# Kernel optimization log

Hardware: AMD Instinct MI355X
Metric: run time of the kernel (lower is better)

Reference implementation:

```python
import jax, jax.numpy as jnp
import numpy as np

# ContextualAttention config (matches init_kwargs)
KS, STRIDE, DIL, FUSE_K, SCALE = 3, 1, 1, 3, 10.0
B, C, H, W = 2, 128, 64, 64
L = H * W  # number of background patches (SAME padding, stride 1)


def _same_pad(x, k, s):
    # TF-style SAME padding, identical to the repo's same_padding helper
    _, _, h, w = x.shape
    oh, ow = -(-h // s), -(-w // s)
    ph = max(0, (oh - 1) * s + k - h)
    pw = max(0, (ow - 1) * s + k - w)
    return jnp.pad(x, ((0, 0), (0, 0), (ph // 2, ph - ph // 2), (pw // 2, pw - pw // 2)))


def _patches(x, k, s):
    # extract_image_patches: SAME pad + unfold -> [N, L, C*k*k], (c, kh, kw) ordering
    xp = _same_pad(x, k, s)
    n, c, hp, wp = xp.shape
    oh, ow = (hp - k) // s + 1, (wp - k) // s + 1
    cols = jnp.stack(
        [xp[:, :, i:i + (oh - 1) * s + 1:s, j:j + (ow - 1) * s + 1:s]
         for i in range(k) for j in range(k)], axis=2)  # [N, C, k*k, oh, ow]
    return cols.reshape(n, c * k * k, oh * ow).transpose(0, 2, 1)


def _fuse(scores):
    # diagonal fuse-smoothing: conv the [L_b, L_f] score matrix with eye(k), twice
    # (second pass on the transposed spatial layout), exactly as in the torch code
    bn = scores.shape[0]
    eye = jnp.eye(FUSE_K, dtype=scores.dtype)[None, None]  # [1,1,k,k]
    conv = lambda v: jax.lax.conv_general_dilated(
        v, eye, (1, 1), [(1, 1), (1, 1)],
        dimension_numbers=('NCHW', 'OIHW', 'NCHW'))
    y = conv(scores.reshape(bn, 1, L, L))
    y = y.reshape(bn, H, W, H, W).transpose(0, 2, 1, 4, 3).reshape(bn, 1, L, L)
    y = conv(y)
    y = y.reshape(bn, W, H, W, H).transpose(0, 2, 1, 4, 3)  # back to [b,H,W,H,W]
    return y.reshape(bn, L, H, W)


def setup_inputs() -> dict:
    key = jax.random.key(0)
    kf, kb, km = jax.random.split(key, 3)
    f = jax.random.normal(kf, (B, C, H, W), jnp.float32)
    b = jax.random.normal(kb, (B, C, H, W), jnp.float32)
    mask = (jax.random.uniform(km, (1, 1, H, W)) < 0.05).astype(jnp.float32)
    return {"f": f, "b": b, "mask": mask}


def reference(f, b, mask):
    kernel = 2 * DIL  # raw patch size for aggregation (=2)
    # raw background patches used by the transposed-conv aggregation
    raw_w = _patches(b, kernel, DIL * STRIDE).reshape(B, L, C, kernel, kernel)
    # DIL == 1 => F.interpolate(scale=1.0, nearest) is identity on f/b/mask
    w = _patches(b, KS, STRIDE)      # [B, L, C*9] matching patches
    fp = _patches(f, KS, 1)          # [B, Lf, C*9] foreground patches (SAME pad)
    m = _patches(mask, KS, STRIDE)[0]                    # [L, 9]
    mm = (jnp.mean(m, axis=1) == 0.0).astype(f.dtype)    # [L] 1 = patch usable

    # per-patch L2 normalization (clamped at 1e-4), conv-as-similarity == patch GEMM
    wn = w / jnp.maximum(jnp.sqrt(jnp.sum(w * w, axis=2, keepdims=True)), 1e-4)
    scores = jnp.einsum('bkd,bqd->bkq', wn, fp).reshape(B, L, H, W)
    scores = _fuse(scores)

    mmb = mm[None, :, None, None]
    attn = jax.nn.softmax(scores * mmb * SCALE, axis=1) * mmb  # softmax over L

    # conv_transpose2d(attn, raw_w, stride=1, padding=1) == VALID corr with flipped,
    # IO-swapped 2x2 kernel (k-1-p = 0 padding); per-sample weights -> vmap
    def agg(a, rw):  # a: [L,H,W], rw: [L,C,2,2]
        rhs = jnp.flip(rw, axis=(2, 3)).transpose(1, 0, 2, 3)  # [C, L, 2, 2] OIHW
        return jax.lax.conv_general_dilated(
            a[None], rhs, (1, 1), [(0, 0), (0, 0)],
            dimension_numbers=('NCHW', 'OIHW', 'NCHW'))[0]

    y = jax.vmap(agg)(attn, raw_w) / 4.0       # [B, C, H-1, W-1]
    y = jnp.pad(y, ((0, 0), (0, 0), (0, 1), (0, 1)))  # output_padding = DIL % 2 = 1
    return y
```

## Files before the change

### kernel.cpp

```cpp
#include <hip/hip_runtime.h>

#define L 4096
#define HH 64
#define CC 128
#define BB 2

typedef _Float16 f16;
typedef _Float16 f16x8 __attribute__((ext_vector_type(8)));
typedef float f32x4 __attribute__((ext_vector_type(4)));

__device__ __forceinline__ void gl_lds16(const f16* g, f16* l) {
  __builtin_amdgcn_global_load_lds(
      (const __attribute__((address_space(1))) void*)g,
      (__attribute__((address_space(3))) void*)l, 16, 0, 0);
}

__device__ __forceinline__ int sigma_(int j) { return ((j & 63) << 6) | (j >> 6); }

__device__ float fuse9(const f16* __restrict__ Sb, int k, int j) {
  float acc = 0.f;
  int cK = sigma_(k), cQ = sigma_(j);
#pragma unroll
  for (int u = -1; u <= 1; ++u) {
    int a = cK + u, bq = cQ + u;
    if ((unsigned)a < L && (unsigned)bq < L) {
      int r = sigma_(a), c = sigma_(bq);
#pragma unroll
      for (int t = -1; t <= 1; ++t) {
        int rr = r + t, cc = c + t;
        if ((unsigned)rr < L && (unsigned)cc < L) acc += (float)Sb[(size_t)rr * L + cc];
      }
    }
  }
  return acc;
}

__global__ __launch_bounds__(256) void k_repack(
    const float* __restrict__ b, const float* __restrict__ f,
    f16* __restrict__ bT, f16* __restrict__ fT, f16* __restrict__ zp) {
  __shared__ float tile[128][65];
  int u0 = blockIdx.x * 64;
  int z = blockIdx.y;
  int batch = z >> 1;
  const float* src = ((z & 1) ? f : b) + (size_t)batch * CC * L;
  f16* dst = ((z & 1) ? fT : bT) + (size_t)batch * L * CC;
  int tid = threadIdx.x;
  if (blockIdx.x == 0 && z == 0 && tid < 32) zp[tid] = (f16)0.f;
#pragma unroll
  for (int i = 0; i < 32; ++i) {
    int idx = i * 256 + tid;
    int c = idx >> 6, ux = idx & 63;
    tile[c][ux] = src[(size_t)c * L + u0 + ux];
  }
  __syncthreads();
#pragma unroll
  for (int j = 0; j < 4; ++j) {
    int t2 = j * 256 + tid;
    int u = t2 >> 4, ch = t2 & 15;
    f16x8 v;
#pragma unroll
    for (int e = 0; e < 8; ++e) v[e] = (f16)tile[ch * 8 + e][u];
    *(f16x8*)(dst + (size_t)(u0 + u) * CC + ch * 8) = v;
  }
}

__global__ __launch_bounds__(256) void k_ssq(const float* __restrict__ b, float* __restrict__ ssq) {
  int u = blockIdx.x * 256 + threadIdx.x;
  int batch = blockIdx.y;
  const float* bp = b + (size_t)batch * CC * L + u;
  float s = 0.f;
#pragma unroll 4
  for (int c = 0; c < CC; ++c) { float v = bp[(size_t)c * L]; s += v * v; }
  ssq[batch * L + u] = s;
}

__global__ void k_norm(const float* __restrict__ ssq, float* __restrict__ inv_n) {
  int gi = blockIdx.x * 256 + threadIdx.x;
  if (gi >= BB * L) return;
  int batch = gi >> 12, k = gi & (L - 1);
  int ky = k >> 6, kx = k & 63;
  float s = 0.f;
#pragma unroll
  for (int dy = -1; dy <= 1; ++dy)
#pragma unroll
    for (int dx = -1; dx <= 1; ++dx) {
      if ((unsigned)(ky + dy) < 64 && (unsigned)(kx + dx) < 64)
        s += ssq[batch * L + k + dy * 64 + dx];
    }
  inv_n[gi] = 1.f / fmaxf(sqrtf(s), 1e-4f);
}

__global__ __launch_bounds__(256) void k_prep_bm(const float* __restrict__ b, f16* __restrict__ bm) {
  int idx = blockIdx.x * 256 + threadIdx.x;
  int e8 = idx * 8;
  int k0 = e8 & (L - 1);
  int c = (e8 >> 12) & (CC - 1);
  int bt = e8 >> 19;
  int batch = bt & 1;
  int tap = bt >> 1;
  int di = 1 - (tap >> 1), dj = 1 - (tap & 1);
  int ky = k0 >> 6, kx0 = k0 & 63;
  const float* src = b + ((size_t)batch * CC + c) * L + k0 + di * 64 + dj;
  bool rowok = (ky + di) < 64;
  f16x8 v;
#pragma unroll
  for (int e = 0; e < 8; ++e) {
    float x = (rowok && (kx0 + e + dj) < 64) ? src[e] : 0.f;
    v[e] = (f16)x;
  }
  *(f16x8*)(bm + (size_t)e8) = v;
}

__global__ void k_prep_mm(const float* __restrict__ mask, float* __restrict__ mmv) {
  int k = blockIdx.x * 256 + threadIdx.x;
  if (k >= L) return;
  int ky = k >> 6, kx = k & 63;
  float s = 0.f;
  for (int i = 0; i < 3; ++i)
    for (int j = 0; j < 3; ++j) {
      int yy = ky + i - 1, xx = kx + j - 1;
      if (yy >= 0 && yy < 64 && xx >= 0 && xx < 64) s += mask[yy * 64 + xx];
    }
  mmv[k] = (s == 0.f) ? 1.f : 0.f;
}

__global__ __launch_bounds__(256) void k_gemm_scores(
    const f16* __restrict__ bT, const f16* __restrict__ fT,
    const float* __restrict__ inv_n, const f16* __restrict__ zp,
    f16* __restrict__ S) {
  __shared__ f16 As[2][128 * 64];
  __shared__ f16 Bs[2][128 * 64];
  int qt = blockIdx.x, kt = blockIdx.y, batch = blockIdx.z;
  int tid = threadIdx.x, wid = tid >> 6, lane = tid & 63;
  int wr = wid >> 1, wc = wid & 1;
  const f16* A0 = bT + (size_t)batch * L * CC;
  const f16* B0 = fT + (size_t)batch * L * CC;
  f32x4 acc[4][4] = {};
  int rA = wr * 64 + (lane & 15);
  int rB = wc * 64 + (lane & 15);

  const f16* baseA_[4]; const f16* baseB_[4];
  int offL_[4];
  unsigned mA_[4], mB_[4];
#pragma unroll
  for (int i = 0; i < 4; ++i) {
    int chunk = (i * 4 + wid) * 64 + lane;
    int row = chunk >> 3;
    int lg = (lane & 7) ^ (row & 7);
    int k = kt * 128 + row;
    int q = qt * 128 + row;
    baseA_[i] = A0 + (size_t)k * CC + lg * 8;
    baseB_[i] = B0 + (size_t)q * CC + lg * 8;
    offL_[i] = chunk * 8;
    int ky = k >> 6, kx = k & 63, qy = q >> 6, qx = q & 63;
    unsigned ma = 0, mb = 0;
#pragma unroll
    for (int rr = 0; rr < 9; ++rr) {
      int dy = rr / 3 - 1, dx = rr - (rr / 3) * 3 - 1;
      if ((unsigned)(ky + dy) < 64u && (unsigned)(kx + dx) < 64u) ma |= 1u << rr;
      if ((unsigned)(qy + dy) < 64u && (unsigned)(qx + dx) < 64u) mb |= 1u << rr;
    }
    mA_[i] = ma; mB_[i] = mb;
  }

#define STAGE_T(tt, bsel)                                                     \
  do {                                                                        \
    int rr_ = (tt) >> 1, half_ = (tt) & 1;                                    \
    int dy_ = rr_ / 3 - 1, dx_ = rr_ - (rr_ / 3) * 3 - 1;                     \
    int doff_ = (dy_ * 64 + dx_) * CC + half_ * 64;                           \
    _Pragma("unroll")                                                         \
    for (int i = 0; i < 4; ++i) {                                             \
      gl_lds16(((mA_[i] >> rr_) & 1u) ? (baseA_[i] + doff_) : zp,             \
               &As[bsel][0] + offL_[i]);                                      \
      gl_lds16(((mB_[i] >> rr_) & 1u) ? (baseB_[i] + doff_) : zp,             \
               &Bs[bsel][0] + offL_[i]);                                      \
    }                                                                         \
  } while (0)

  STAGE_T(0, 0);
  int cur = 0;
#pragma unroll 1
  for (int t = 0; t < 18; ++t) {
    __syncthreads();
    if (t < 17) STAGE_T(t + 1, cur ^ 1);
    const f16* Ab = &As[cur][0];
    const f16* Bb = &Bs[cur][0];
#pragma unroll
    for (int h2 = 0; h2 < 2; ++h2) {
      int cb = h2 * 4 + (lane >> 4);
      f16x8 af[4], bf[4];
#pragma unroll
      for (int m = 0; m < 4; ++m) {
        int row = rA + m * 16;
        af[m] = *(const f16x8*)(Ab + row * 64 + ((cb ^ (row & 7)) * 8));
      }
#pragma unroll
      for (int n = 0; n < 4; ++n) {
        int row = rB + n * 16;
        bf[n] = *(const f16x8*)(Bb + row * 64 + ((cb ^ (row & 7)) * 8));
      }
#pragma unroll
      for (int m = 0; m < 4; ++m)
#pragma unroll
        for (int n = 0; n < 4; ++n)
          acc[m][n] = __builtin_amdgcn_mfma_f32_16x16x32_f16(af[m], bf[n], acc[m][n], 0, 0, 0);
    }
    cur ^= 1;
  }
#undef STAGE_T

  f16* Srow = S + (size_t)batch * L * L;
  int kbase = kt * 128 + wr * 64 + (lane >> 4) * 4;
  int qbase = qt * 128 + wc * 64 + (lane & 15);
#pragma unroll
  for (int m = 0; m < 4; ++m) {
    f32x4 invv = *(const f32x4*)(inv_n + (size_t)batch * L + kbase + m * 16);
#pragma unroll
    for (int r = 0; r < 4; ++r) {
      f16* dst = Srow + (size_t)(kbase + m * 16 + r) * L + qbase;
#pragma unroll
      for (int n = 0; n < 4; ++n) dst[n * 16] = (f16)(acc[m][n][r] * invv[r]);
    }
  }
}

__global__ __launch_bounds__(256) void k_fuse_stats(
    const f16* __restrict__ S, const float* __restrict__ mmv,
    float* __restrict__ T3, float* __restrict__ pm, float* __restrict__ pl) {
  int tid = threadIdx.x;
  if (tid >= 247) return;
  int jc = blockIdx.x, kc = blockIdx.y, batch = blockIdx.z;
  int g = jc * 247 + tid;
  int q0 = 72 + g * 8;
  const f16* Sb = S + (size_t)batch * L * L;
  float* Tb = T3 + (size_t)batch * L * L;
  float m8[8], l8[8];
#pragma unroll
  for (int e = 0; e < 8; ++e) { m8[e] = -3.0e38f; l8[e] = 0.f; }
  int cnt = 0;
  int k0 = kc * 16;
  for (int kk = 0; kk < 16; ++kk) {
    int k = k0 + kk;
    if (mmv[k] == 0.f) { ++cnt; continue; }
    float acc[8] = {0.f, 0.f, 0.f, 0.f, 0.f, 0.f, 0.f, 0.f};
    int cK = sigma_(k);
#pragma unroll
    for (int u = -1; u <= 1; ++u) {
      int a = cK + u;
      if ((unsigned)a >= L) continue;
      int r = sigma_(a);
      const f16* cb = Sb + (size_t)r * L + (q0 + 64 * u);
      {
        f16x8 v = *(const f16x8*)cb;
#pragma unroll
        for (int e = 0; e < 8; ++e) acc[e] += (float)v[e];
      }
      if (r >= 1) {
        const f16* rm = cb - L;
        f16x8 v = *(const f16x8*)rm;
        acc[0] += (float)rm[-1];
#pragma unroll
        for (int e = 1; e < 8; ++e) acc[e] += (float)v[e - 1];
      }
      if (r <= L - 2) {
        const f16* rp = cb + L;
        f16x8 v = *(const f16x8*)rp;
#pragma unroll
        for (int e = 0; e < 7; ++e) acc[e] += (float)v[e + 1];
        acc[7] += (float)rp[8];
      }
    }
#pragma unroll
    for (int e = 0; e < 8; ++e) acc[e] *= 10.f;
    float* trow = Tb + (size_t)k * L + q0;
    *(f32x4*)trow = *(f32x4*)&acc[0];
    *(f32x4*)(trow + 4) = *(f32x4*)&acc[4];
#pragma unroll
    for (int e = 0; e < 8; ++e) {
      float nm = fmaxf(m8[e], acc[e]);
      l8[e] = l8[e] * __expf(m8[e] - nm) + __expf(acc[e] - nm);
      m8[e] = nm;
    }
  }
  float fc = (float)cnt;
  float om[8], ol[8];
#pragma unroll
  for (int e = 0; e < 8; ++e) {
    float nm = fmaxf(m8[e], 0.f);
    ol[e] = l8[e] * __expf(m8[e] - nm) + fc * __expf(-nm);
    om[e] = nm;
  }
  float* pmp = pm + (size_t)kc * (BB * L) + (size_t)batch * L + q0;
  float* plp = pl + (size_t)kc * (BB * L) + (size_t)batch * L + q0;
  *(f32x4*)pmp = *(f32x4*)&om[0]; *(f32x4*)(pmp + 4) = *(f32x4*)&om[4];
  *(f32x4*)plp = *(f32x4*)&ol[0]; *(f32x4*)(plp + 4) = *(f32x4*)&ol[4];
}

__global__ __launch_bounds__(256) void k_fuse_stats_edge(
    const f16* __restrict__ S, const float* __restrict__ mmv,
    float* __restrict__ T3, float* __restrict__ pm, float* __restrict__ pl) {
  int tid = threadIdx.x;
  if (tid >= 144) return;
  int q = (tid < 72) ? tid : (4024 + tid - 72);
  int kc = blockIdx.x, batch = blockIdx.y;
  const f16* Sb = S + (size_t)batch * L * L;
  float* Tb = T3 + (size_t)batch * L * L;
  float m = -3.0e38f, l = 0.f;
  int cnt = 0;
  int k0 = kc * 16;
  for (int kk = 0; kk < 16; ++kk) {
    int k = k0 + kk;
    if (mmv[k] == 0.f) { ++cnt; continue; }
    float logit = 10.f * fuse9(Sb, k, q);
    Tb[(size_t)k * L + q] = logit;
    float nm = fmaxf(m, logit);
    l = l * __expf(m - nm) + __expf(logit - nm);
    m = nm;
  }
  float nm = fmaxf(m, 0.f);
  l = l * __expf(m - nm) + (float)cnt * __expf(-nm);
  pm[(size_t)kc * (BB * L) + (size_t)batch * L + q] = nm;
  pl[(size_t)kc * (BB * L) + (size_t)batch * L + q] = l;
}

__global__ __launch_bounds__(256) void k_softmax_reduce(
    const float* __restrict__ pm, const float* __restrict__ pl,
    float* __restrict__ Mq, float* __restrict__ invLq) {
  __shared__ float sm[4][64], sl[4][64];
  int tid = threadIdx.x;
  int ql = tid & 63, part = tid >> 6;
  int qi = blockIdx.x * 64 + ql;
  float m = -3.0e38f, l = 0.f;
  int i0 = part * 64;
#pragma unroll 4
  for (int i = i0; i < i0 + 64; ++i) {
    float pmv = pm[(size_t)i * (BB * L) + qi];
    float plv = pl[(size_t)i * (BB * L) + qi];
    float nm = fmaxf(m, pmv);
    l = l * __expf(m - nm) + plv * __expf(pmv - nm);
    m = nm;
  }
  sm[part][ql] = m; sl[part][ql] = l;
  __syncthreads();
  if (part == 0) {
    float M = sm[0][ql];
#pragma unroll
    for (int p = 1; p < 4; ++p) M = fmaxf(M, sm[p][ql]);
    float Ls = 0.f;
#pragma unroll
    for (int p = 0; p < 4; ++p) Ls += sl[p][ql] * __expf(sm[p][ql] - M);
    Mq[qi] = M;
    invLq[qi] = 1.f / Ls;
  }
}

__global__ __launch_bounds__(512) void k_agg(
    const float* __restrict__ T3, const float* __restrict__ mmv,
    const float* __restrict__ Mq, const float* __restrict__ invLq,
    const f16* __restrict__ bm, float* __restrict__ part) {
  __shared__ f16 Asm[512 * 32];
  __shared__ f16 Bt[136 * 40];
  int pt = blockIdx.x, ks = blockIdx.y, batch = blockIdx.z;
  int p0 = pt * 64;
  int tid = threadIdx.x, wid = tid >> 6, lane = tid & 63;
  int wr = wid >> 1, wc = wid & 1;
  const float* Tb = T3 + (size_t)batch * L * L;

  const f16* gA_[4]; f16* lA_[4];
#pragma unroll
  for (int i = 0; i < 4; ++i) {
    int R = wid * 64 + i * 16 + (lane >> 2);
    int tap = R >> 7, c = R & 127;
    int chl = (lane & 3) ^ ((R >> 1) & 3);
    gA_[i] = bm + (((size_t)(tap * 2 + batch) * CC + c) * L) + chl * 8;
    lA_[i] = Asm + R * 32 + (lane & 3) * 8;
  }

  bool act1 = (tid < 32);
  int pp_[2], kg_[2]; bool qok_[2]; float M_[2], iL_[2];
  const float* tb_[2]; f16* bw_[2];
#pragma unroll
  for (int s = 0; s < 2; ++s) {
    int tau = tid + s * 512;
    int ppv = tau % 136, kgv = tau / 136;
    if (tau >= 544) { ppv = 0; kgv = 0; }
    pp_[s] = ppv; kg_[s] = kgv;
    int q = p0 + ppv;
    bool qok = q < L;
    int qc = qok ? q : (L - 1);
    qok_[s] = qok;
    M_[s] = Mq[(size_t)batch * L + qc];
    iL_[s] = invLq[(size_t)batch * L + qc];
    tb_[s] = Tb + (size_t)(kgv * 8) * L + qc;
    bw_[s] = Bt + ppv * 40 + ((kgv ^ ((ppv >> 3) & 3)) * 8);
  }

  f16x8 vv_[2];
  int kend = ks * 1024 + 1024;

#define LOADB(K0)                                                             \
  do {                                                                        \
    _Pragma("unroll")                                                         \
    for (int s = 0; s < 2; ++s) {                                             \
      if (s == 1 && !act1) break;                                             \
      const float* tp = tb_[s] + (size_t)(K0) * L;                            \
      f32x4 ma = *(const f32x4*)(mmv + (K0) + kg_[s] * 8);                    \
      f32x4 mb = *(const f32x4*)(mmv + (K0) + kg_[s] * 8 + 4);                \
      float t[8];                                                             \
      _Pragma("unroll")                                                       \
      for (int j = 0; j < 8; ++j) t[j] = tp[(size_t)j * L];                   \
      f16 v[8];                                                               \
      _Pragma("unroll")                                                       \
      for (int j = 0; j < 8; ++j) {                                           \
        float mmj = (j < 4) ? ma[j] : mb[j - 4];                              \
        v[j] = (qok_[s] && mmj != 0.f)                                        \
                   ? (f16)(__expf(t[j] - M_[s]) * iL_[s]) : (f16)0.f;         \
      }                                                                       \
      vv_[s] = *(f16x8*)v;                                                    \
    }                                                                         \
  } while (0)

  LOADB(ks * 1024);
  f32x4 acc[2][2] = {};
#pragma unroll 1
  for (int k0 = ks * 1024; k0 < kend; k0 += 32) {
    __syncthreads();
    *(f16x8*)bw_[0] = vv_[0];
    if (act1) *(f16x8*)bw_[1] = vv_[1];
#pragma unroll
    for (int i = 0; i < 4; ++i) gl_lds16(gA_[i] + k0, lA_[i]);
    __syncthreads();
#pragma unroll
    for (int tap = 0; tap < 4; ++tap) {
      int dlt = (tap >> 1) * 64 + (tap & 1);
      f16x8 af[2], bf[2];
#pragma unroll
      for (int m = 0; m < 2; ++m) {
        int R = tap * 128 + wr * 32 + m * 16 + (lane & 15);
        int ph = (lane >> 4) ^ ((R >> 1) & 3);
        af[m] = *(const f16x8*)(Asm + R * 32 + ph * 8);
      }
#pragma unroll
      for (int n = 0; n < 2; ++n) {
        int pp = wc * 32 + n * 16 + (lane & 15) + dlt;
        int ph = (lane >> 4) ^ ((pp >> 3) & 3);
        bf[n] = *(const f16x8*)(Bt + pp * 40 + ph * 8);
      }
#pragma unroll
      for (int m = 0; m < 2; ++m)
#pragma unroll
        for (int n = 0; n < 2; ++n)
          acc[m][n] = __builtin_amdgcn_mfma_f32_16x16x32_f16(af[m], bf[n], acc[m][n], 0, 0, 0);
    }
    if (k0 + 32 < kend) LOADB(k0 + 32);
  }
#undef LOADB

  int cb = wr * 32 + (lane >> 4) * 4;
  int pb = p0 + wc * 32 + (lane & 15);
#pragma unroll
  for (int m = 0; m < 2; ++m)
#pragma unroll
    for (int n = 0; n < 2; ++n)
#pragma unroll
      for (int r = 0; r < 4; ++r) {
        int c = cb + m * 16 + r;
        int p = pb + n * 16;
        part[(((size_t)ks * 2 + batch) * CC + c) * L + p] = acc[m][n][r];
      }
}

__global__ __launch_bounds__(256) void k_agg_reduce(const float* __restrict__ part, float* __restrict__ out) {
  int idx = (blockIdx.x * 256 + threadIdx.x) * 4;
  f32x4 s = {0.f, 0.f, 0.f, 0.f};
#pragma unroll
  for (int ks = 0; ks < 4; ++ks) {
    f32x4 v = *(const f32x4*)(part + (size_t)ks * (2 * CC * L) + idx);
#pragma unroll
    for (int e = 0; e < 4; ++e) s[e] += v[e];
  }
  int p = idx & (L - 1);
  int u = p >> 6, vv = p & 63;
  f32x4 o;
#pragma unroll
  for (int e = 0; e < 4; ++e) o[e] = (u < 63 && (vv + e) < 63) ? s[e] * 0.25f : 0.f;
  *(f32x4*)(out + idx) = o;
}

extern "C" void kernel_launch(void* const* d_in, const int* in_sizes, int n_in,
                              void* d_out, int out_size, void* d_ws, size_t ws_size,
                              hipStream_t stream) {
  const float* f = (const float*)d_in[0];
  const float* b = (const float*)d_in[1];
  const float* mask = (const float*)d_in[2];
  float* out = (float*)d_out;
  char* ws = (char*)d_ws;

  float* T3  = (float*)(ws + 0);
  f16* S     = (f16*)(ws + 134217728);
  f16* bm    = (f16*)(ws + 201326592);
  float* part= (float*)(ws + 209715200);
  float* pm  = (float*)(ws + 226492416);
  float* pl  = (float*)(ws + 234881024);
  float* mmv = (float*)(ws + 243269632);
  float* Mq  = (float*)(ws + 243286016);
  float* iLq = (float*)(ws + 243318784);
  f16* bT    = (f16*)(ws + 243351552);
  f16* fT    = (f16*)(ws + 245448704);
  float* ssq = (float*)(ws + 247545856);
  float* invn= (float*)(ws + 247578624);
  f16* zp    = (f16*)(ws + 247611392);

  k_repack<<<dim3(64, 4), dim3(256), 0, stream>>>(b, f, bT, fT, zp);
  k_ssq<<<dim3(16, 2), dim3(256), 0, stream>>>(b, ssq);
  k_norm<<<dim3(32), dim3(256), 0, stream>>>(ssq, invn);
  k_prep_bm<<<dim3(2048), dim3(256), 0, stream>>>(b, bm);
  k_prep_mm<<<dim3(16), dim3(256), 0, stream>>>(mask, mmv);
  k_gemm_scores<<<dim3(32, 32, 2), dim3(256), 0, stream>>>(bT, fT, invn, zp, S);
  k_fuse_stats<<<dim3(2, 256, 2), dim3(256), 0, stream>>>(S, mmv, T3, pm, pl);
  k_fuse_stats_edge<<<dim3(256, 2), dim3(256), 0, stream>>>(S, mmv, T3, pm, pl);
  k_softmax_reduce<<<dim3(128), dim3(256), 0, stream>>>(pm, pl, Mq, iLq);
  k_agg<<<dim3(64, 4, 2), dim3(512), 0, stream>>>(T3, mmv, Mq, iLq, bm, part);
  k_agg_reduce<<<dim3(1024), dim3(256), 0, stream>>>(part, out);
}
```

Before: 321.1 us.

## Store chunk-local softmax exponentials as fp16 instead of fp32 logits

The fuse-stats kernels now compute exp(logit - chunk max) over 8-row k chunks and store these probabilities as fp16 P, replacing the full fp32 logit matrix T3. This halves the largest intermediate's write and read traffic. The aggregation kernel rescales each value by exp(chunk max - global max)/sum, so it no longer needs a per-element exp. Masked-row counts move to a small zcnt kernel used in the softmax reduce. The trade-offs are fp16 rounding of the unnormalised probabilities, twice as many partial-stat chunks to reduce, and an extra per-chunk pm load in the aggregation loop.

Measured after the change: 310.4 us. 1.03x faster.

```diff
diff --git a/kernel.cpp b/kernel.cpp
--- a/kernel.cpp
+++ b/kernel.cpp
@@ -122,6 +122,15 @@
       if (yy >= 0 && yy < 64 && xx >= 0 && xx < 64) s += mask[yy * 64 + xx];
     }
   mmv[k] = (s == 0.f) ? 1.f : 0.f;
+}
+
+__global__ void k_zcnt(const float* __restrict__ mmv, float* __restrict__ zcnt) {
+  int i = blockIdx.x * 256 + threadIdx.x;
+  if (i >= 512) return;
+  float s = 0.f;
+#pragma unroll
+  for (int r = 0; r < 8; ++r) s += (mmv[i * 8 + r] == 0.f) ? 1.f : 0.f;
+  zcnt[i] = s;
 }
 
 __global__ __launch_bounds__(256) void k_gemm_scores(
@@ -226,22 +235,25 @@
 
 __global__ __launch_bounds__(256) void k_fuse_stats(
     const f16* __restrict__ S, const float* __restrict__ mmv,
-    float* __restrict__ T3, float* __restrict__ pm, float* __restrict__ pl) {
+    f16* __restrict__ P, float* __restrict__ pmP, float* __restrict__ pl) {
   int tid = threadIdx.x;
   if (tid >= 247) return;
   int jc = blockIdx.x, kc = blockIdx.y, batch = blockIdx.z;
   int g = jc * 247 + tid;
   int q0 = 72 + g * 8;
   const f16* Sb = S + (size_t)batch * L * L;
-  float* Tb = T3 + (size_t)batch * L * L;
-  float m8[8], l8[8];
-#pragma unroll
-  for (int e = 0; e < 8; ++e) { m8[e] = -3.0e38f; l8[e] = 0.f; }
-  int cnt = 0;
-  int k0 = kc * 16;
-  for (int kk = 0; kk < 16; ++kk) {
+  f16* Pb = P + (size_t)batch * L * L;
+  float lg[8][8];
+  float m8[8];
+#pragma unroll
+  for (int e = 0; e < 8; ++e) m8[e] = -3.0e38f;
+  unsigned vmask = 0;
+  int k0 = kc * 8;
+#pragma unroll
+  for (int kk = 0; kk < 8; ++kk) {
     int k = k0 + kk;
-    if (mmv[k] == 0.f) { ++cnt; continue; }
+    if (mmv[k] == 0.f) continue;
+    vmask |= 1u << kk;
     float acc[8] = {0.f, 0.f, 0.f, 0.f, 0.f, 0.f, 0.f, 0.f};
     int cK = sigma_(k);
 #pragma unroll
@@ -271,74 +283,89 @@
       }
     }
 #pragma unroll
-    for (int e = 0; e < 8; ++e) acc[e] *= 10.f;
-    float* trow = Tb + (size_t)k * L + q0;
-    *(f32x4*)trow = *(f32x4*)&acc[0];
-    *(f32x4*)(trow + 4) = *(f32x4*)&acc[4];
-#pragma unroll
     for (int e = 0; e < 8; ++e) {
-      float nm = fmaxf(m8[e], acc[e]);
-      l8[e] = l8[e] * __expf(m8[e] - nm) + __expf(acc[e] - nm);
-      m8[e] = nm;
-    }
-  }
-  float fc = (float)cnt;
-  float om[8], ol[8];
-#pragma unroll
-  for (int e = 0; e < 8; ++e) {
-    float nm = fmaxf(m8[e], 0.f);
-    ol[e] = l8[e] * __expf(m8[e] - nm) + fc * __expf(-nm);
-    om[e] = nm;
-  }
-  float* pmp = pm + (size_t)kc * (BB * L) + (size_t)batch * L + q0;
+      float x = acc[e] * 10.f;
+      lg[kk][e] = x;
+      m8[e] = fmaxf(m8[e], x);
+    }
+  }
+  float l8[8] = {0.f, 0.f, 0.f, 0.f, 0.f, 0.f, 0.f, 0.f};
+#pragma unroll
+  for (int kk = 0; kk < 8; ++kk) {
+    if (!((vmask >> kk) & 1u)) continue;
+    f16 v[8];
+#pragma unroll
+    for (int e = 0; e < 8; ++e) {
+      float p = __expf(lg[kk][e] - m8[e]);
+      l8[e] += p;
+      v[e] = (f16)p;
+    }
+    *(f16x8*)(Pb + (size_t)(k0 + kk) * L + q0) = *(f16x8*)v;
+  }
+  float* pmp = pmP + (size_t)kc * (BB * L) + (size_t)batch * L + q0;
   float* plp = pl + (size_t)kc * (BB * L) + (size_t)batch * L + q0;
-  *(f32x4*)pmp = *(f32x4*)&om[0]; *(f32x4*)(pmp + 4) = *(f32x4*)&om[4];
-  *(f32x4*)plp = *(f32x4*)&ol[0]; *(f32x4*)(plp + 4) = *(f32x4*)&ol[4];
+  *(f32x4*)pmp = *(f32x4*)&m8[0]; *(f32x4*)(pmp + 4) = *(f32x4*)&m8[4];
+  *(f32x4*)plp = *(f32x4*)&l8[0]; *(f32x4*)(plp + 4) = *(f32x4*)&l8[4];
 }
 
 __global__ __launch_bounds__(256) void k_fuse_stats_edge(
     const f16* __restrict__ S, const float* __restrict__ mmv,
-    float* __restrict__ T3, float* __restrict__ pm, float* __restrict__ pl) {
+    f16* __restrict__ P, float* __restrict__ pmP, float* __restrict__ pl) {
   int tid = threadIdx.x;
   if (tid >= 144) return;
   int q = (tid < 72) ? tid : (4024 + tid - 72);
   int kc = blockIdx.x, batch = blockIdx.y;
   const f16* Sb = S + (size_t)batch * L * L;
-  float* Tb = T3 + (size_t)batch * L * L;
-  float m = -3.0e38f, l = 0.f;
-  int cnt = 0;
-  int k0 = kc * 16;
-  for (int kk = 0; kk < 16; ++kk) {
+  f16* Pb = P + (size_t)batch * L * L;
+  float lgs[8];
+  float m = -3.0e38f;
+  unsigned vmask = 0;
+  int k0 = kc * 8;
+#pragma unroll
+  for (int kk = 0; kk < 8; ++kk) {
     int k = k0 + kk;
-    if (mmv[k] == 0.f) { ++cnt; continue; }
-    float logit = 10.f * fuse9(Sb, k, q);
-    Tb[(size_t)k * L + q] = logit;
-    float nm = fmaxf(m, logit);
-    l = l * __expf(m - nm) + __expf(logit - nm);
-    m = nm;
-  }
-  float nm = fmaxf(m, 0.f);
-  l = l * __expf(m - nm) + (float)cnt * __expf(-nm);
-  pm[(size_t)kc * (BB * L) + (size_t)batch * L + q] = nm;
+    if (mmv[k] == 0.f) continue;
+    vmask |= 1u << kk;
+    float x = 10.f * fuse9(Sb, k, q);
+    lgs[kk] = x;
+    m = fmaxf(m, x);
+  }
+  float l = 0.f;
+#pragma unroll
+  for (int kk = 0; kk < 8; ++kk) {
+    if (!((vmask >> kk) & 1u)) continue;
+    float p = __expf(lgs[kk] - m);
+    l += p;
+    Pb[(size_t)(k0 + kk) * L + q] = (f16)p;
+  }
+  pmP[(size_t)kc * (BB * L) + (size_t)batch * L + q] = m;
   pl[(size_t)kc * (BB * L) + (size_t)batch * L + q] = l;
 }
 
 __global__ __launch_bounds__(256) void k_softmax_reduce(
-    const float* __restrict__ pm, const float* __restrict__ pl,
+    const float* __restrict__ pmP, const float* __restrict__ pl,
+    const float* __restrict__ zcnt,
     float* __restrict__ Mq, float* __restrict__ invLq) {
   __shared__ float sm[4][64], sl[4][64];
   int tid = threadIdx.x;
   int ql = tid & 63, part = tid >> 6;
   int qi = blockIdx.x * 64 + ql;
   float m = -3.0e38f, l = 0.f;
-  int i0 = part * 64;
+  int i0 = part * 128;
+  float cntp = 0.f;
 #pragma unroll 4
-  for (int i = i0; i < i0 + 64; ++i) {
-    float pmv = pm[(size_t)i * (BB * L) + qi];
+  for (int i = i0; i < i0 + 128; ++i) {
+    float pmv = pmP[(size_t)i * (BB * L) + qi];
     float plv = pl[(size_t)i * (BB * L) + qi];
     float nm = fmaxf(m, pmv);
     l = l * __expf(m - nm) + plv * __expf(pmv - nm);
     m = nm;
+    cntp += zcnt[i & 511];
+  }
+  if (cntp > 0.f) {
+    float nm = fmaxf(m, 0.f);
+    l = l * __expf(m - nm) + cntp * __expf(-nm);
+    m = nm;
   }
   sm[part][ql] = m; sl[part][ql] = l;
   __syncthreads();
@@ -355,7 +382,8 @@
 }
 
 __global__ __launch_bounds__(512) void k_agg(
-    const float* __restrict__ T3, const float* __restrict__ mmv,
+    const f16* __restrict__ P, const float* __restrict__ pmP,
+    const float* __restrict__ mmv,
     const float* __restrict__ Mq, const float* __restrict__ invLq,
     const f16* __restrict__ bm, float* __restrict__ part) {
   __shared__ f16 Asm[512 * 32];
@@ -364,7 +392,7 @@
   int p0 = pt * 64;
   int tid = threadIdx.x, wid = tid >> 6, lane = tid & 63;
   int wr = wid >> 1, wc = wid & 1;
-  const float* Tb = T3 + (size_t)batch * L * L;
+  const f16* Pb = P + (size_t)batch * L * L;
 
   const f16* gA_[4]; f16* lA_[4];
 #pragma unroll
@@ -377,21 +405,23 @@
   }
 
   bool act1 = (tid < 32);
-  int pp_[2], kg_[2]; bool qok_[2]; float M_[2], iL_[2];
-  const float* tb_[2]; f16* bw_[2];
+  int kg_[2]; bool qok_[2]; float M_[2], iL_[2];
+  const f16* tb_[2]; f16* bw_[2];
+  size_t bq_[2];
 #pragma unroll
   for (int s = 0; s < 2; ++s) {
     int tau = tid + s * 512;
     int ppv = tau % 136, kgv = tau / 136;
     if (tau >= 544) { ppv = 0; kgv = 0; }
-    pp_[s] = ppv; kg_[s] = kgv;
+    kg_[s] = kgv;
     int q = p0 + ppv;
     bool qok = q < L;
     int qc = qok ? q : (L - 1);
     qok_[s] = qok;
     M_[s] = Mq[(size_t)batch * L + qc];
     iL_[s] = invLq[(size_t)batch * L + qc];
-    tb_[s] = Tb + (size_t)(kgv * 8) * L + qc;
+    tb_[s] = Pb + (size_t)(kgv * 8) * L + qc;
+    bq_[s] = (size_t)batch * L + qc;
     bw_[s] = Bt + ppv * 40 + ((kgv ^ ((ppv >> 3) & 3)) * 8);
   }
 
@@ -403,18 +433,20 @@
     _Pragma("unroll")                                                         \
     for (int s = 0; s < 2; ++s) {                                             \
       if (s == 1 && !act1) break;                                             \
-      const float* tp = tb_[s] + (size_t)(K0) * L;                            \
+      const f16* tp = tb_[s] + (size_t)(K0) * L;                              \
+      int ck = ((K0) >> 3) + kg_[s];                                          \
+      float pmv = pmP[(size_t)ck * (BB * L) + bq_[s]];                        \
+      float corr = qok_[s] ? __expf(pmv - M_[s]) * iL_[s] : 0.f;              \
       f32x4 ma = *(const f32x4*)(mmv + (K0) + kg_[s] * 8);                    \
       f32x4 mb = *(const f32x4*)(mmv + (K0) + kg_[s] * 8 + 4);                \
-      float t[8];                                                             \
+      f16 pv[8];                                                              \
       _Pragma("unroll")                                                       \
-      for (int j = 0; j < 8; ++j) t[j] = tp[(size_t)j * L];                   \
+      for (int j = 0; j < 8; ++j) pv[j] = tp[(size_t)j * L];                  \
       f16 v[8];                                                               \
       _Pragma("unroll")                                                       \
       for (int j = 0; j < 8; ++j) {                                           \
         float mmj = (j < 4) ? ma[j] : mb[j - 4];                              \
-        v[j] = (qok_[s] && mmj != 0.f)                                        \
-                   ? (f16)(__expf(t[j] - M_[s]) * iL_[s]) : (f16)0.f;         \
+        v[j] = (mmj != 0.f) ? (f16)((float)pv[j] * corr) : (f16)0.f;          \
       }                                                                       \
       vv_[s] = *(f16x8*)v;                                                    \
     }                                                                         \
@@ -496,30 +528,32 @@
   float* out = (float*)d_out;
   char* ws = (char*)d_ws;
 
-  float* T3  = (float*)(ws + 0);
-  f16* S     = (f16*)(ws + 134217728);
-  f16* bm    = (f16*)(ws + 201326592);
-  float* part= (float*)(ws + 209715200);
-  float* pm  = (float*)(ws + 226492416);
-  float* pl  = (float*)(ws + 234881024);
-  float* mmv = (float*)(ws + 243269632);
-  float* Mq  = (float*)(ws + 243286016);
-  float* iLq = (float*)(ws + 243318784);
-  f16* bT    = (f16*)(ws + 243351552);
-  f16* fT    = (f16*)(ws + 245448704);
-  float* ssq = (float*)(ws + 247545856);
-  float* invn= (float*)(ws + 247578624);
-  f16* zp    = (f16*)(ws + 247611392);
+  f16* P     = (f16*)(ws + 0);
+  f16* S     = (f16*)(ws + 67108864);
+  f16* bm    = (f16*)(ws + 134217728);
+  float* part= (float*)(ws + 142606336);
+  float* pmP = (float*)(ws + 159383552);
+  float* pl  = (float*)(ws + 176160768);
+  float* mmv = (float*)(ws + 192937984);
+  float* Mq  = (float*)(ws + 192954368);
+  float* iLq = (float*)(ws + 192987136);
+  f16* bT    = (f16*)(ws + 193019904);
+  f16* fT    = (f16*)(ws + 195117056);
+  float* ssq = (float*)(ws + 197214208);
+  float* invn= (float*)(ws + 197246976);
+  f16* zp    = (f16*)(ws + 197279744);
+  float* zcnt= (float*)(ws + 197279872);
 
   k_repack<<<dim3(64, 4), dim3(256), 0, stream>>>(b, f, bT, fT, zp);
   k_ssq<<<dim3(16, 2), dim3(256), 0, stream>>>(b, ssq);
   k_norm<<<dim3(32), dim3(256), 0, stream>>>(ssq, invn);
   k_prep_bm<<<dim3(2048), dim3(256), 0, stream>>>(b, bm);
   k_prep_mm<<<dim3(16), dim3(256), 0, stream>>>(mask, mmv);
+  k_zcnt<<<dim3(2), dim3(256), 0, stream>>>(mmv, zcnt);
   k_gemm_scores<<<dim3(32, 32, 2), dim3(256), 0, stream>>>(bT, fT, invn, zp, S);
-  k_fuse_stats<<<dim3(2, 256, 2), dim3(256), 0, stream>>>(S, mmv, T3, pm, pl);
-  k_fuse_stats_edge<<<dim3(256, 2), dim3(256), 0, stream>>>(S, mmv, T3, pm, pl);
-  k_softmax_reduce<<<dim3(128), dim3(256), 0, stream>>>(pm, pl, Mq, iLq);
-  k_agg<<<dim3(64, 4, 2), dim3(512), 0, stream>>>(T3, mmv, Mq, iLq, bm, part);
+  k_fuse_stats<<<dim3(2, 512, 2), dim3(256), 0, stream>>>(S, mmv, P, pmP, pl);
+  k_fuse_stats_edge<<<dim3(512, 2), dim3(256), 0, stream>>>(S, mmv, P, pmP, pl);
+  k_softmax_reduce<<<dim3(128), dim3(256), 0, stream>>>(pmP, pl, zcnt, Mq, iLq);
+  k_agg<<<dim3(64, 4, 2), dim3(512), 0, stream>>>(P, pmP, mmv, Mq, iLq, bm, part);
   k_agg_reduce<<<dim3(1024), dim3(256), 0, stream>>>(part, out);
 }
```
